# Optimization experiments

Hardware: AMD Instinct MI355X
Metric: run time of the kernel (lower is better)

Reference implementation:

```python
import jax, jax.numpy as jnp
import numpy as np
from jax import lax

V, D, L, H = 8000, 512, 8, 8
B, PROMPT, NEW = 16, 64, 16
T = PROMPT + NEW
PAD, EOS = 0, 3
HD = D // H


def setup_inputs() -> dict:
    key = jax.random.key(0)
    ks = jax.random.split(key, 10)
    s = 0.02
    p = {}
    p['wte'] = jax.random.normal(ks[0], (V, D), jnp.float32) * s
    p['wpe'] = jax.random.normal(ks[1], (T, D), jnp.float32) * s
    p['ln1_w'] = jnp.ones((L, D), jnp.float32)
    p['ln1_b'] = jnp.zeros((L, D), jnp.float32)
    p['qkv_w'] = jax.random.normal(ks[2], (L, D, 3 * D), jnp.float32) * s
    p['qkv_b'] = jnp.zeros((L, 3 * D), jnp.float32)
    p['ao_w'] = jax.random.normal(ks[3], (L, D, D), jnp.float32) * s
    p['ao_b'] = jnp.zeros((L, D), jnp.float32)
    p['ln2_w'] = jnp.ones((L, D), jnp.float32)
    p['ln2_b'] = jnp.zeros((L, D), jnp.float32)
    p['fc_w'] = jax.random.normal(ks[4], (L, D, 4 * D), jnp.float32) * s
    p['fc_b'] = jnp.zeros((L, 4 * D), jnp.float32)
    p['pr_w'] = jax.random.normal(ks[5], (L, 4 * D, D), jnp.float32) * s
    p['pr_b'] = jnp.zeros((L, D), jnp.float32)
    p['lnf_w'] = jnp.ones((D,), jnp.float32)
    p['lnf_b'] = jnp.zeros((D,), jnp.float32)
    p['lm_w'] = jax.random.normal(ks[6], (D, V), jnp.float32) * s
    prompt = jax.random.randint(ks[7], (B, PROMPT), 4, V).astype(jnp.int32)
    p['input_ids'] = jnp.concatenate([prompt, jnp.full((B, NEW), PAD, jnp.int32)], axis=1)
    p['attention_mask'] = jnp.broadcast_to((jnp.arange(T) < PROMPT).astype(jnp.int32), (B, T))
    p['max_new_tokens'] = NEW
    return p


def _ln(x, w, b):
    m = x.mean(-1, keepdims=True)
    v = ((x - m) ** 2).mean(-1, keepdims=True)
    return (x - m) / jnp.sqrt(v + 1e-5) * w + b


def reference(wte, wpe, ln1_w, ln1_b, qkv_w, qkv_b, ao_w, ao_b, ln2_w, ln2_b,
              fc_w, fc_b, pr_w, pr_b, lnf_w, lnf_b, lm_w,
              input_ids, attention_mask, max_new_tokens):
    Bsz, Tlen = input_ids.shape
    causal = jnp.tril(jnp.ones((Tlen, Tlen), bool))
    bidx = jnp.arange(Bsz)
    layer_params = (ln1_w, ln1_b, qkv_w, qkv_b, ao_w, ao_b, ln2_w, ln2_b, fc_w, fc_b, pr_w, pr_b)
    scale = 1.0 / np.sqrt(HD).astype(np.float32)

    def fwd(ids, msk):
        # Full dense forward over the whole (padded) prefix, as the teacher does each step.
        x = wte[ids] + wpe[None, :Tlen]
        bias = jnp.where(causal[None, None] & (msk[:, None, None, :] > 0), 0.0, -1e9)
        def block(x, p):
            l1w, l1b, qw, qb, aw, ab, l2w, l2b, fw, fb, pw, pb = p
            h = _ln(x, l1w, l1b)
            qkv = h @ qw + qb                                  # [B,T,3D]
            q, k, v = jnp.split(qkv, 3, axis=-1)
            def heads(t):
                return t.reshape(Bsz, Tlen, H, HD).transpose(0, 2, 1, 3)
            q, k, v = heads(q), heads(k), heads(v)
            s = jnp.einsum('bhqd,bhkd->bhqk', q, k) * scale + bias
            o = jnp.einsum('bhqk,bhkd->bhqd', jax.nn.softmax(s, axis=-1), v)
            o = o.transpose(0, 2, 1, 3).reshape(Bsz, Tlen, D)
            x = x + o @ aw + ab
            h2 = _ln(x, l2w, l2b)
            x = x + jax.nn.gelu(h2 @ fw + fb) @ pw + pb
            return x, None
        x, _ = lax.scan(block, x, layer_params)
        x = _ln(x, lnf_w, lnf_b)
        return x @ lm_w                                        # [B,T,V]

    lengths = attention_mask.sum(-1).astype(jnp.int32)
    carry0 = (input_ids, attention_mask, lengths,
              jnp.zeros(Bsz, bool), jnp.zeros(Bsz, jnp.float32), jnp.zeros(Bsz, jnp.float32))

    def step(carry, _):
        ids, msk, lens, fin, csum, ccnt = carry
        logits = fwd(ids, msk)
        last = jnp.clip(lens - 1, 0, Tlen - 1)
        sl = logits[bidx, last].astype(jnp.float32)            # [B,V]
        probs = jax.nn.softmax(sl, axis=-1)
        top_id = jnp.argmax(sl, axis=-1).astype(jnp.int32)
        top_p = jnp.max(probs, axis=-1)
        active = (~fin) & (lens < Tlen)
        csum = csum + jnp.where(active, top_p, 0.0)
        ccnt = ccnt + active.astype(jnp.float32)
        is_end = (top_id == EOS) | (top_id == PAD)
        write = active & (~is_end)
        pos = jnp.clip(lens, 0, Tlen - 1)
        ids = ids.at[bidx, pos].set(jnp.where(write, top_id, ids[bidx, pos]))
        msk = msk.at[bidx, pos].set(jnp.where(write, 1, msk[bidx, pos]))
        lens = lens + write.astype(jnp.int32)
        fin = fin | (active & is_end)
        tok = jnp.where(write, top_id, PAD)                    # generated token this step (PAD if none)
        return (ids, msk, lens, fin, csum, ccnt), tok

    carry, toks = lax.scan(step, carry0, None, length=max_new_tokens)
    _, _, _, _, csum, ccnt = carry
    generated = toks.T                                         # [B, max_new_tokens]
    confidences = csum / jnp.maximum(ccnt, 1.0)
    return generated, confidences
```

## Files before the change

### kernel.cpp

```cpp
#include <hip/hip_runtime.h>
#include <math.h>

#define VOCAB 8000
#define DIM 512
#define NLAYER 8
#define NHEAD 8
#define BATCH 16
#define TMAX 80
#define PROMPT_LEN 64
#define NNEW 16
#define HEADD 64
#define ATT_SCALE 0.125f

#define SRC_PLAIN 0
#define SRC_LN 1
#define SRC_GELU 2

__device__ __forceinline__ float gelu_f(float x) {
  return 0.5f * x * (1.0f + tanhf(0.7978845608028654f * (x + 0.044715f * x * x * x)));
}

__global__ void k_init(const int* __restrict__ ids_in, const int* __restrict__ mask_in,
                       int* __restrict__ ids, int* __restrict__ lens, int* __restrict__ fin,
                       float* __restrict__ csum, float* __restrict__ ccnt) {
  int tid = threadIdx.x;
  for (int i = tid; i < BATCH * TMAX; i += blockDim.x) ids[i] = ids_in[i];
  if (tid < BATCH) {
    int s = 0;
    for (int t = 0; t < TMAX; ++t) s += mask_in[tid * TMAX + t];
    lens[tid] = s;
    fin[tid] = 0;
    csum[tid] = 0.f;
    ccnt[tid] = 0.f;
  }
}

__global__ void k_embed_prefill(const int* __restrict__ ids, const float* __restrict__ wte,
                                const float* __restrict__ wpe, float* __restrict__ x) {
  int bt = blockIdx.x;
  int b = bt / PROMPT_LEN, t = bt % PROMPT_LEN;
  int tok = ids[b * TMAX + t];
  for (int d = threadIdx.x; d < DIM; d += blockDim.x)
    x[(size_t)bt * DIM + d] = wte[(size_t)tok * DIM + d] + wpe[(size_t)t * DIM + d];
}

__global__ void k_layernorm(const float* __restrict__ x, const float* __restrict__ w,
                            const float* __restrict__ b, float* __restrict__ out) {
  int row = blockIdx.x;
  int tid = threadIdx.x;
  const float* xr = x + (size_t)row * DIM;
  __shared__ float red[256];
  float v0 = xr[tid], v1 = xr[tid + 256];
  red[tid] = v0 + v1;
  __syncthreads();
  for (int s = 128; s > 0; s >>= 1) {
    if (tid < s) red[tid] += red[tid + s];
    __syncthreads();
  }
  float mean = red[0] * (1.0f / DIM);
  __syncthreads();
  float d0 = v0 - mean, d1 = v1 - mean;
  red[tid] = d0 * d0 + d1 * d1;
  __syncthreads();
  for (int s = 128; s > 0; s >>= 1) {
    if (tid < s) red[tid] += red[tid + s];
    __syncthreads();
  }
  float rstd = 1.0f / sqrtf(red[0] * (1.0f / DIM) + 1e-5f);
  out[(size_t)row * DIM + tid] = d0 * rstd * w[tid] + b[tid];
  out[(size_t)row * DIM + tid + 256] = d1 * rstd * w[tid + 256] + b[tid + 256];
}

template <int MODE>
__global__ __launch_bounds__(256) void gemm_kernel(const float* __restrict__ A,
                                                   const float* __restrict__ W,
                                                   const float* __restrict__ bias,
                                                   const float* __restrict__ res,
                                                   float* __restrict__ C, int M, int N, int K,
                                                   float* __restrict__ kcT,
                                                   float* __restrict__ vc) {
  const int BM = 64, BN = 64, BK = 16;
  __shared__ float As[BK][BM + 4];
  __shared__ float Ws[BK][BN];
  int tid = threadIdx.x;
  int bm = blockIdx.y * BM, bn = blockIdx.x * BN;
  int tr = tid / 16, tc = tid % 16;
  float acc[4][4];
#pragma unroll
  for (int i = 0; i < 4; i++)
#pragma unroll
    for (int j = 0; j < 4; j++) acc[i][j] = 0.f;

  for (int k0 = 0; k0 < K; k0 += BK) {
    for (int i = tid; i < BM * BK; i += 256) {
      int m = i / BK, kk = i % BK;
      As[kk][m] = A[(size_t)(bm + m) * K + k0 + kk];
    }
    for (int i = tid; i < BK * BN; i += 256) {
      int kk = i / BN, n = i % BN;
      Ws[kk][n] = W[(size_t)(k0 + kk) * N + bn + n];
    }
    __syncthreads();
#pragma unroll
    for (int kk = 0; kk < BK; ++kk) {
      float a[4], w[4];
#pragma unroll
      for (int i = 0; i < 4; i++) a[i] = As[kk][tr * 4 + i];
#pragma unroll
      for (int j = 0; j < 4; j++) w[j] = Ws[kk][tc * 4 + j];
#pragma unroll
      for (int i = 0; i < 4; i++)
#pragma unroll
        for (int j = 0; j < 4; j++) acc[i][j] += a[i] * w[j];
    }
    __syncthreads();
  }
#pragma unroll
  for (int i = 0; i < 4; i++) {
    int m = bm + tr * 4 + i;
#pragma unroll
    for (int j = 0; j < 4; j++) {
      int n = bn + tc * 4 + j;
      float v = acc[i][j] + (bias ? bias[n] : 0.f);
      if (MODE == 1) v = gelu_f(v);
      if (MODE == 2) v += res[(size_t)m * N + n];
      if (MODE == 3) {
        int b = m >> 6, t = m & 63;
        if (n < DIM) {
          C[(size_t)m * N + n] = v;
        } else if (n < 2 * DIM) {
          int dd = n - DIM;
          kcT[((size_t)(b * NHEAD + (dd >> 6)) * HEADD + (dd & 63)) * TMAX + t] = v;
        } else {
          int dd = n - 2 * DIM;
          vc[((size_t)(b * NHEAD + (dd >> 6)) * TMAX + t) * HEADD + (dd & 63)] = v;
        }
      } else {
        C[(size_t)m * N + n] = v;
      }
    }
  }
}

__global__ void k_attn_prefill(const float* __restrict__ qkv, const float* __restrict__ kcT,
                               const float* __restrict__ vc, float* __restrict__ o) {
  int blk = blockIdx.x;
  int q = blk % PROMPT_LEN;
  int bh = blk / PROMPT_LEN;
  int h = bh % NHEAD, b = bh / NHEAD;
  int tid = threadIdx.x;
  __shared__ float qs[HEADD];
  __shared__ float ps[PROMPT_LEN];
  qs[tid] = qkv[(size_t)(b * PROMPT_LEN + q) * 3 * DIM + h * HEADD + tid];
  __syncthreads();
  const float* kbT = kcT + (size_t)(b * NHEAD + h) * HEADD * TMAX;
  const float* vb = vc + (size_t)(b * NHEAD + h) * TMAX * HEADD;
  float s = -1e30f;
  if (tid <= q) {
    float a = 0.f;
    for (int d = 0; d < HEADD; ++d) a += qs[d] * kbT[d * TMAX + tid];
    s = a * ATT_SCALE;
  }
  float mx = s;
  for (int off = 32; off > 0; off >>= 1) mx = fmaxf(mx, __shfl_xor(mx, off));
  float e = (tid <= q) ? expf(s - mx) : 0.f;
  float sum = e;
  for (int off = 32; off > 0; off >>= 1) sum += __shfl_xor(sum, off);
  ps[tid] = e / sum;
  __syncthreads();
  float acc = 0.f;
  for (int t = 0; t <= q; ++t) acc += ps[t] * vb[t * HEADD + tid];
  o[(size_t)(b * PROMPT_LEN + q) * DIM + h * HEADD + tid] = acc;
}

__global__ void k_embed0(const int* __restrict__ ids, const int* __restrict__ lens,
                         const float* __restrict__ wte, const float* __restrict__ wpe,
                         float* __restrict__ xdT) {
  int b = blockIdx.x;
  int p = lens[b] - 1;
  if (p < 0) p = 0;
  if (p > TMAX - 1) p = TMAX - 1;
  int tok = ids[b * TMAX + p];
  for (int d = threadIdx.x; d < DIM; d += blockDim.x)
    xdT[(size_t)d * BATCH + b] = wte[(size_t)tok * DIM + d] + wpe[(size_t)p * DIM + d];
}

template <int KB, int SRC, int P, int LAYOUT, bool BIAS, bool XDW, int N, int K>
__global__ __launch_bounds__(512) void k_skinny(const float* __restrict__ src,
                                                const float* __restrict__ parts,
                                                const float* __restrict__ lnw,
                                                const float* __restrict__ lnb,
                                                const float* __restrict__ bias,
                                                const float* __restrict__ W,
                                                float* __restrict__ out,
                                                float* __restrict__ xdout) {
  constexpr int KRANGE = K / KB;
  constexpr int SROWS = (SRC == SRC_LN) ? K : KRANGE;
  __shared__ float sm[SROWS * BATCH];
  __shared__ float wsum[8][BATCH];
  __shared__ float wss[8][BATCH];
  __shared__ float smean[BATCH], srstd[BATCH];
  const int tid = threadIdx.x;
  const int base_row = (SRC == SRC_LN) ? 0 : blockIdx.y * KRANGE;

  {
    const float4* s4 = (const float4*)src;
    float4* d4 = (float4*)sm;
    constexpr int NF4 = SROWS * BATCH / 4;
    for (int i = tid; i < NF4; i += 512) {
      int gi = base_row * (BATCH / 4) + i;
      float4 v;
      if (SRC == SRC_GELU) {
        v = make_float4(0.f, 0.f, 0.f, 0.f);
      } else {
        v = s4[gi];
      }
#pragma unroll
      for (int p = 0; p < P; ++p) {
        const float4* p4 = (const float4*)(parts + (size_t)p * K * BATCH);
        float4 t = p4[gi];
        v.x += t.x;
        v.y += t.y;
        v.z += t.z;
        v.w += t.w;
      }
      if (SRC == SRC_GELU) {
        v.x = gelu_f(v.x);
        v.y = gelu_f(v.y);
        v.z = gelu_f(v.z);
        v.w = gelu_f(v.w);
      }
      if (XDW) {
        if (blockIdx.x == 0 && blockIdx.y == 0) ((float4*)xdout)[gi] = v;
      }
      d4[i] = v;
    }
  }
  if (SRC == SRC_LN) {
    __syncthreads();
    float s = 0.f, ss = 0.f;
#pragma unroll
    for (int j = 0; j < 16; ++j) {
      float v = sm[tid + 512 * j];
      s += v;
      ss += v * v;
    }
    s += __shfl_xor(s, 16);
    ss += __shfl_xor(ss, 16);
    s += __shfl_xor(s, 32);
    ss += __shfl_xor(ss, 32);
    int lane0 = tid & 63, w0 = tid >> 6;
    if (lane0 < BATCH) {
      wsum[w0][lane0] = s;
      wss[w0][lane0] = ss;
    }
    __syncthreads();
    if (tid < BATCH) {
      float ts = 0.f, tss = 0.f;
#pragma unroll
      for (int ww = 0; ww < 8; ++ww) {
        ts += wsum[ww][tid];
        tss += wss[ww][tid];
      }
      float m = ts * (1.0f / K);
      float var = tss * (1.0f / K) - m * m;
      smean[tid] = m;
      srstd[tid] = 1.0f / sqrtf(var + 1e-5f);
    }
    __syncthreads();
    float mb = smean[tid & 15];
    float rb = srstd[tid & 15];
#pragma unroll
    for (int j = 0; j < 16; ++j) {
      int idx = tid + 512 * j;
      int k = idx >> 4;
      sm[idx] = (sm[idx] - mb) * rb * lnw[k] + lnb[k];
    }
  }
  __syncthreads();

  const int lane = tid & 63;
  const int w = tid >> 6;
  const int bw = w & 1;
  const int kw = w >> 1;
  constexpr int KCH = KRANGE / 4;
  const int col = blockIdx.x * 64 + lane;
  const float* Wp = W + (size_t)(blockIdx.y * KRANGE + kw * KCH) * N + col;
  const int fbase = ((SRC == SRC_LN) ? blockIdx.y * KRANGE : 0) + kw * KCH;
  float acc[8];
#pragma unroll
  for (int i = 0; i < 8; ++i) acc[i] = 0.f;
  for (int k = 0; k < KCH; k += 8) {
    float wv[8];
#pragma unroll
    for (int u = 0; u < 8; ++u) wv[u] = Wp[(size_t)(k + u) * N];
#pragma unroll
    for (int u = 0; u < 8; ++u) {
      const float4* a4 = (const float4*)&sm[(fbase + k + u) * BATCH + bw * 8];
      float4 A0 = a4[0], A1 = a4[1];
      acc[0] = fmaf(A0.x, wv[u], acc[0]);
      acc[1] = fmaf(A0.y, wv[u], acc[1]);
      acc[2] = fmaf(A0.z, wv[u], acc[2]);
      acc[3] = fmaf(A0.w, wv[u], acc[3]);
      acc[4] = fmaf(A1.x, wv[u], acc[4]);
      acc[5] = fmaf(A1.y, wv[u], acc[5]);
      acc[6] = fmaf(A1.z, wv[u], acc[6]);
      acc[7] = fmaf(A1.w, wv[u], acc[7]);
    }
  }
  __syncthreads();
#pragma unroll
  for (int i = 0; i < 8; ++i) sm[(w * 8 + i) * 64 + lane] = acc[i];
  __syncthreads();
  for (int o = tid; o < BATCH * 64; o += 512) {
    int b, gn_l;
    if (LAYOUT == 1) {
      b = o & 15;
      gn_l = o >> 4;
    } else {
      b = o >> 6;
      gn_l = o & 63;
    }
    int bw2 = b >> 3, bi = b & 7;
    float v = 0.f;
#pragma unroll
    for (int k2 = 0; k2 < 4; ++k2) v += sm[(((k2 * 2 + bw2) * 8) + bi) * 64 + gn_l];
    int gn = blockIdx.x * 64 + gn_l;
    if (BIAS && blockIdx.y == 0) v += bias[gn];
    if (KB == 1 && LAYOUT == 0)
      out[(size_t)b * N + gn] = v;
    else if (LAYOUT == 0)
      out[((size_t)blockIdx.y * BATCH + b) * N + gn] = v;
    else
      out[(size_t)blockIdx.y * N * BATCH + (size_t)gn * BATCH + b] = v;
  }
}

__global__ void k_attn_decode(const float* __restrict__ qp, const int* __restrict__ lens,
                              float* __restrict__ kcT, float* __restrict__ vc,
                              float* __restrict__ ot) {
  int h = blockIdx.x % NHEAD, b = blockIdx.x / NHEAD;
  int d = threadIdx.x;
  int p = lens[b] - 1;
  if (p < 0) p = 0;
  if (p > TMAX - 1) p = TMAX - 1;
  const float* q0 = qp + (size_t)b * 3 * DIM + h * HEADD;
  const float* q1 = qp + (size_t)BATCH * 3 * DIM + (size_t)b * 3 * DIM + h * HEADD;
  float qv = q0[d] + q1[d];
  float kself = q0[DIM + d] + q1[DIM + d];
  float vself = q0[2 * DIM + d] + q1[2 * DIM + d];
  float* kT = kcT + (size_t)(b * NHEAD + h) * HEADD * TMAX;
  float* vb = vc + (size_t)(b * NHEAD + h) * TMAX * HEADD;
  kT[d * TMAX + p] = kself;
  vb[p * HEADD + d] = vself;
  __shared__ float qs[HEADD];
  __shared__ float ps[TMAX];
  qs[d] = qv;
  __syncthreads();
  float pd = qv * kself;
  for (int off = 32; off > 0; off >>= 1) pd += __shfl_xor(pd, off);
  float selfdot = pd * ATT_SCALE;
  float s0 = -1e30f, s1 = -1e30f;
  int t1 = d + 64;
  if (d < p) {
    float a = 0.f;
    for (int dd = 0; dd < HEADD; ++dd) a += qs[dd] * kT[dd * TMAX + d];
    s0 = a * ATT_SCALE;
  } else if (d == p) {
    s0 = selfdot;
  }
  if (t1 < p) {
    float a = 0.f;
    for (int dd = 0; dd < HEADD; ++dd) a += qs[dd] * kT[dd * TMAX + t1];
    s1 = a * ATT_SCALE;
  } else if (t1 == p) {
    s1 = selfdot;
  }
  float mx = fmaxf(s0, s1);
  for (int off = 32; off > 0; off >>= 1) mx = fmaxf(mx, __shfl_xor(mx, off));
  float e0 = (d <= p) ? expf(s0 - mx) : 0.f;
  float e1 = (t1 <= p) ? expf(s1 - mx) : 0.f;
  float sum = e0 + e1;
  for (int off = 32; off > 0; off >>= 1) sum += __shfl_xor(sum, off);
  float inv = 1.f / sum;
  ps[d] = e0 * inv;
  if (d < TMAX - 64) ps[t1] = e1 * inv;
  __syncthreads();
  float acc = 0.f;
  for (int t = 0; t < p; ++t) acc += ps[t] * vb[t * HEADD + d];
  acc += ps[p] * vself;
  ot[(size_t)(h * HEADD + d) * BATCH + b] = acc;
}

__global__ __launch_bounds__(512) void k_lnf(const float* __restrict__ xd,
                                             const float* __restrict__ parts,
                                             const float* __restrict__ lnw,
                                             const float* __restrict__ lnb,
                                             float* __restrict__ At) {
  __shared__ float sm[DIM * BATCH];
  __shared__ float wsum[8][BATCH];
  __shared__ float wss[8][BATCH];
  __shared__ float smean[BATCH], srstd[BATCH];
  const int tid = threadIdx.x;
  {
    const float4* s4 = (const float4*)xd;
    float4* d4 = (float4*)sm;
    for (int i = tid; i < DIM * BATCH / 4; i += 512) {
      float4 v = s4[i];
#pragma unroll
      for (int p = 0; p < 4; ++p) {
        const float4* p4 = (const float4*)(parts + (size_t)p * DIM * BATCH);
        float4 t = p4[i];
        v.x += t.x;
        v.y += t.y;
        v.z += t.z;
        v.w += t.w;
      }
      d4[i] = v;
    }
  }
  __syncthreads();
  float s = 0.f, ss = 0.f;
#pragma unroll
  for (int j = 0; j < 16; ++j) {
    float v = sm[tid + 512 * j];
    s += v;
    ss += v * v;
  }
  s += __shfl_xor(s, 16);
  ss += __shfl_xor(ss, 16);
  s += __shfl_xor(s, 32);
  ss += __shfl_xor(ss, 32);
  int lane0 = tid & 63, w0 = tid >> 6;
  if (lane0 < BATCH) {
    wsum[w0][lane0] = s;
    wss[w0][lane0] = ss;
  }
  __syncthreads();
  if (tid < BATCH) {
    float ts = 0.f, tss = 0.f;
#pragma unroll
    for (int ww = 0; ww < 8; ++ww) {
      ts += wsum[ww][tid];
      tss += wss[ww][tid];
    }
    float m = ts * (1.0f / DIM);
    float var = tss * (1.0f / DIM) - m * m;
    smean[tid] = m;
    srstd[tid] = 1.0f / sqrtf(var + 1e-5f);
  }
  __syncthreads();
  float mb = smean[tid & 15];
  float rb = srstd[tid & 15];
#pragma unroll
  for (int j = 0; j < 16; ++j) {
    int idx = tid + 512 * j;
    int k = idx >> 4;
    At[idx] = (sm[idx] - mb) * rb * lnw[k] + lnb[k];
  }
}

__global__ void k_update(const float* __restrict__ logits, int* __restrict__ ids,
                         int* __restrict__ lens, int* __restrict__ fin, float* __restrict__ csum,
                         float* __restrict__ ccnt, float* __restrict__ out_gen, int step,
                         const float* __restrict__ wte, const float* __restrict__ wpe,
                         float* __restrict__ xdT) {
  int b = blockIdx.x, tid = threadIdx.x;
  const float* lr = logits + (size_t)b * VOCAB;
  __shared__ float vred[256];
  __shared__ int ired[256];
  __shared__ int sh_tok, sh_pos;
  float best = -1e30f;
  int besti = 0;
  for (int i = tid; i < VOCAB; i += 256) {
    float v = lr[i];
    if (v > best) {
      best = v;
      besti = i;
    }
  }
  vred[tid] = best;
  ired[tid] = besti;
  __syncthreads();
  for (int s = 128; s > 0; s >>= 1) {
    if (tid < s) {
      if (vred[tid + s] > vred[tid] ||
          (vred[tid + s] == vred[tid] && ired[tid + s] < ired[tid])) {
        vred[tid] = vred[tid + s];
        ired[tid] = ired[tid + s];
      }
    }
    __syncthreads();
  }
  float mx = vred[0];
  int top = ired[0];
  __syncthreads();
  float se = 0.f;
  for (int i = tid; i < VOCAB; i += 256) se += expf(lr[i] - mx);
  vred[tid] = se;
  __syncthreads();
  for (int s = 128; s > 0; s >>= 1) {
    if (tid < s) vred[tid] += vred[tid + s];
    __syncthreads();
  }
  if (tid == 0) {
    float top_p = 1.f / vred[0];
    int l = lens[b];
    bool active = (!fin[b]) && (l < TMAX);
    if (active) {
      csum[b] += top_p;
      ccnt[b] += 1.f;
    }
    bool is_end = (top == 3) || (top == 0);
    bool wr = active && !is_end;
    if (wr) {
      ids[b * TMAX + l] = top;
      lens[b] = l + 1;
    }
    if (active && is_end) fin[b] = 1;
    out_gen[b * NNEW + step] = wr ? (float)top : 0.f;
    int l2 = lens[b];
    int pn = l2 - 1;
    if (pn < 0) pn = 0;
    if (pn > TMAX - 1) pn = TMAX - 1;
    sh_pos = pn;
    sh_tok = ids[b * TMAX + pn];
  }
  __syncthreads();
  int tok = sh_tok, pn = sh_pos;
  xdT[(size_t)tid * BATCH + b] = wte[(size_t)tok * DIM + tid] + wpe[(size_t)pn * DIM + tid];
  xdT[(size_t)(tid + 256) * BATCH + b] =
      wte[(size_t)tok * DIM + tid + 256] + wpe[(size_t)pn * DIM + tid + 256];
}

__global__ void k_finalize(const float* __restrict__ csum, const float* __restrict__ ccnt,
                           float* __restrict__ out) {
  int b = threadIdx.x;
  if (b < BATCH) out[BATCH * NNEW + b] = csum[b] / fmaxf(ccnt[b], 1.f);
}

extern "C" void kernel_launch(void* const* d_in, const int* in_sizes, int n_in, void* d_out,
                              int out_size, void* d_ws, size_t ws_size, hipStream_t stream) {
  const float* wte = (const float*)d_in[0];
  const float* wpe = (const float*)d_in[1];
  const float* ln1_w = (const float*)d_in[2];
  const float* ln1_b = (const float*)d_in[3];
  const float* qkv_w = (const float*)d_in[4];
  const float* qkv_b = (const float*)d_in[5];
  const float* ao_w = (const float*)d_in[6];
  const float* ao_b = (const float*)d_in[7];
  const float* ln2_w = (const float*)d_in[8];
  const float* ln2_b = (const float*)d_in[9];
  const float* fc_w = (const float*)d_in[10];
  const float* fc_b = (const float*)d_in[11];
  const float* pr_w = (const float*)d_in[12];
  const float* pr_b = (const float*)d_in[13];
  const float* lnf_w = (const float*)d_in[14];
  const float* lnf_b = (const float*)d_in[15];
  const float* lm_w = (const float*)d_in[16];
  const int* ids_in = (const int*)d_in[17];
  const int* mask_in = (const int*)d_in[18];
  float* out = (float*)d_out;

  char* p = (char*)d_ws;
  auto carve = [&](size_t nbytes) {
    char* r = p;
    p += (nbytes + 255) & ~(size_t)255;
    return (void*)r;
  };
  int* w_ids = (int*)carve(BATCH * TMAX * 4);
  int* w_lens = (int*)carve(BATCH * 4);
  int* w_fin = (int*)carve(BATCH * 4);
  float* w_csum = (float*)carve(BATCH * 4);
  float* w_ccnt = (float*)carve(BATCH * 4);
  float* w_x = (float*)carve((size_t)BATCH * PROMPT_LEN * DIM * 4);
  float* w_h = (float*)carve((size_t)BATCH * PROMPT_LEN * DIM * 4);
  float* w_qkv = (float*)carve((size_t)BATCH * PROMPT_LEN * 3 * DIM * 4);
  float* w_att = (float*)carve((size_t)BATCH * PROMPT_LEN * DIM * 4);
  float* w_mlp = (float*)carve((size_t)BATCH * PROMPT_LEN * 4 * DIM * 4);
  float* w_kc = (float*)carve((size_t)NLAYER * BATCH * NHEAD * TMAX * HEADD * 4);
  float* w_vc = (float*)carve((size_t)NLAYER * BATCH * NHEAD * TMAX * HEADD * 4);
  float* w_xd0 = (float*)carve((size_t)DIM * BATCH * 4);
  float* w_xd1 = (float*)carve((size_t)DIM * BATCH * 4);
  float* w_at = (float*)carve((size_t)DIM * BATCH * 4);
  float* w_ot = (float*)carve((size_t)DIM * BATCH * 4);
  float* w_qkp = (float*)carve((size_t)2 * BATCH * 3 * DIM * 4);
  float* w_aop = (float*)carve((size_t)2 * DIM * BATCH * 4);
  float* w_fcp = (float*)carve((size_t)2 * 4 * DIM * BATCH * 4);
  float* w_prp = (float*)carve((size_t)4 * DIM * BATCH * 4);
  float* w_logits = (float*)carve((size_t)BATCH * VOCAB * 4);

  const int M = BATCH * PROMPT_LEN;
  const size_t kvstride = (size_t)BATCH * NHEAD * TMAX * HEADD;

  k_init<<<1, 256, 0, stream>>>(ids_in, mask_in, w_ids, w_lens, w_fin, w_csum, w_ccnt);
  k_embed_prefill<<<M, 256, 0, stream>>>(w_ids, wte, wpe, w_x);

  for (int l = 0; l < NLAYER; ++l) {
    float* kc = w_kc + (size_t)l * kvstride;
    float* vc = w_vc + (size_t)l * kvstride;
    k_layernorm<<<M, 256, 0, stream>>>(w_x, ln1_w + l * DIM, ln1_b + l * DIM, w_h);
    gemm_kernel<3><<<dim3(3 * DIM / 64, M / 64), 256, 0, stream>>>(
        w_h, qkv_w + (size_t)l * DIM * 3 * DIM, qkv_b + (size_t)l * 3 * DIM, nullptr, w_qkv, M,
        3 * DIM, DIM, kc, vc);
    k_attn_prefill<<<BATCH * NHEAD * PROMPT_LEN, 64, 0, stream>>>(w_qkv, kc, vc, w_att);
    gemm_kernel<2><<<dim3(DIM / 64, M / 64), 256, 0, stream>>>(
        w_att, ao_w + (size_t)l * DIM * DIM, ao_b + (size_t)l * DIM, w_x, w_x, M, DIM, DIM,
        nullptr, nullptr);
    k_layernorm<<<M, 256, 0, stream>>>(w_x, ln2_w + l * DIM, ln2_b + l * DIM, w_h);
    gemm_kernel<1><<<dim3(4 * DIM / 64, M / 64), 256, 0, stream>>>(
        w_h, fc_w + (size_t)l * DIM * 4 * DIM, fc_b + (size_t)l * 4 * DIM, nullptr, w_mlp, M,
        4 * DIM, DIM, nullptr, nullptr);
    gemm_kernel<2><<<dim3(DIM / 64, M / 64), 256, 0, stream>>>(
        w_mlp, pr_w + (size_t)l * 4 * DIM * DIM, pr_b + (size_t)l * DIM, w_x, w_x, M, DIM,
        4 * DIM, nullptr, nullptr);
  }

  k_embed0<<<BATCH, 256, 0, stream>>>(w_ids, w_lens, wte, wpe, w_xd0);

  for (int s = 0; s < NNEW; ++s) {
    for (int l = 0; l < NLAYER; ++l) {
      float* kc = w_kc + (size_t)l * kvstride;
      float* vc = w_vc + (size_t)l * kvstride;
      if (l == 0) {
        k_skinny<2, SRC_LN, 0, 0, true, false, 3 * DIM, DIM>
            <<<dim3(24, 2), 512, 0, stream>>>(w_xd0, nullptr, ln1_w + l * DIM, ln1_b + l * DIM,
                                              qkv_b + (size_t)l * 3 * DIM,
                                              qkv_w + (size_t)l * DIM * 3 * DIM, w_qkp, nullptr);
      } else {
        k_skinny<2, SRC_LN, 4, 0, true, true, 3 * DIM, DIM>
            <<<dim3(24, 2), 512, 0, stream>>>(w_xd1, w_prp, ln1_w + l * DIM, ln1_b + l * DIM,
                                              qkv_b + (size_t)l * 3 * DIM,
                                              qkv_w + (size_t)l * DIM * 3 * DIM, w_qkp, w_xd0);
      }
      k_attn_decode<<<BATCH * NHEAD, 64, 0, stream>>>(w_qkp, w_lens, kc, vc, w_ot);
      k_skinny<2, SRC_PLAIN, 0, 1, true, false, DIM, DIM><<<dim3(8, 2), 512, 0, stream>>>(
          w_ot, nullptr, nullptr, nullptr, ao_b + (size_t)l * DIM, ao_w + (size_t)l * DIM * DIM,
          w_aop, nullptr);
      k_skinny<2, SRC_LN, 2, 1, true, true, 4 * DIM, DIM><<<dim3(32, 2), 512, 0, stream>>>(
          w_xd0, w_aop, ln2_w + l * DIM, ln2_b + l * DIM, fc_b + (size_t)l * 4 * DIM,
          fc_w + (size_t)l * DIM * 4 * DIM, w_fcp, w_xd1);
      k_skinny<4, SRC_GELU, 2, 1, true, false, DIM, 4 * DIM><<<dim3(8, 4), 512, 0, stream>>>(
          nullptr, w_fcp, nullptr, nullptr, pr_b + (size_t)l * DIM,
          pr_w + (size_t)l * 4 * DIM * DIM, w_prp, nullptr);
    }
    k_lnf<<<1, 512, 0, stream>>>(w_xd1, w_prp, lnf_w, lnf_b, w_at);
    k_skinny<1, SRC_PLAIN, 0, 0, false, false, VOCAB, DIM><<<dim3(VOCAB / 64, 1), 512, 0, stream>>>(
        w_at, nullptr, nullptr, nullptr, nullptr, lm_w, w_logits, nullptr);
    k_update<<<BATCH, 256, 0, stream>>>(w_logits, w_ids, w_lens, w_fin, w_csum, w_ccnt, out, s,
                                        wte, wpe, w_xd0);
  }
  k_finalize<<<1, 64, 0, stream>>>(w_csum, w_ccnt, out);
}
```

Baseline: 12.21 ms.

## Fuse decode loop into persistent kernel with atomic grid barriers

Replaces the roughly 100 per-step decode kernel launches with one persistent 128-block kernel. Stages are separated by a software grid barrier built on an atomic counter. Final layernorm is folded into the LM-head GEMM, and attention packs 8 heads per block. This removes launch and inter-kernel gaps, but relies on all 128 blocks being co-resident and adds barrier spin cost.

Result: slower. 21.81 ms (+78.7%).

```diff
diff --git a/kernel.cpp b/kernel.cpp
--- a/kernel.cpp
+++ b/kernel.cpp
@@ -16,15 +16,19 @@
 #define SRC_LN 1
 #define SRC_GELU 2
 
+#define GRIDN 128
+
 __device__ __forceinline__ float gelu_f(float x) {
   return 0.5f * x * (1.0f + tanhf(0.7978845608028654f * (x + 0.044715f * x * x * x)));
 }
 
 __global__ void k_init(const int* __restrict__ ids_in, const int* __restrict__ mask_in,
                        int* __restrict__ ids, int* __restrict__ lens, int* __restrict__ fin,
-                       float* __restrict__ csum, float* __restrict__ ccnt) {
+                       float* __restrict__ csum, float* __restrict__ ccnt,
+                       unsigned long long* __restrict__ bar) {
   int tid = threadIdx.x;
   for (int i = tid; i < BATCH * TMAX; i += blockDim.x) ids[i] = ids_in[i];
+  if (tid == 0) *bar = 0ull;
   if (tid < BATCH) {
     int s = 0;
     for (int t = 0; t < TMAX; ++t) s += mask_in[tid * TMAX + t];
@@ -173,35 +177,55 @@
   o[(size_t)(b * PROMPT_LEN + q) * DIM + h * HEADD + tid] = acc;
 }
 
-__global__ void k_embed0(const int* __restrict__ ids, const int* __restrict__ lens,
-                         const float* __restrict__ wte, const float* __restrict__ wpe,
-                         float* __restrict__ xdT) {
-  int b = blockIdx.x;
-  int p = lens[b] - 1;
-  if (p < 0) p = 0;
-  if (p > TMAX - 1) p = TMAX - 1;
-  int tok = ids[b * TMAX + p];
-  for (int d = threadIdx.x; d < DIM; d += blockDim.x)
-    xdT[(size_t)d * BATCH + b] = wte[(size_t)tok * DIM + d] + wpe[(size_t)p * DIM + d];
+
+struct SmGemm {
+  float sm[DIM * BATCH];
+  float wsum[8][BATCH];
+  float wss[8][BATCH];
+  float smean[BATCH], srstd[BATCH];
+};
+struct SmAttn {
+  float qs[8][HEADD];
+  float ps[8][TMAX];
+};
+struct SmUpd {
+  float vred[512];
+  int ired[512];
+  int sh_tok, sh_pos;
+};
+union SmAll {
+  SmGemm g;
+  SmAttn a;
+  SmUpd u;
+};
+
+__device__ __forceinline__ void gsync(unsigned long long* bar) {
+  __syncthreads();
+  if (threadIdx.x == 0) {
+    unsigned long long arr =
+        __hip_atomic_fetch_add(bar, 1ull, __ATOMIC_RELEASE, __HIP_MEMORY_SCOPE_AGENT);
+    unsigned long long target = (arr / GRIDN + 1ull) * (unsigned long long)GRIDN;
+    while (__hip_atomic_load(bar, __ATOMIC_RELAXED, __HIP_MEMORY_SCOPE_AGENT) < target)
+      __builtin_amdgcn_s_sleep(2);
+    __threadfence();
+  }
+  __syncthreads();
 }
 
 template <int KB, int SRC, int P, int LAYOUT, bool BIAS, bool XDW, int N, int K>
-__global__ __launch_bounds__(512) void k_skinny(const float* __restrict__ src,
-                                                const float* __restrict__ parts,
-                                                const float* __restrict__ lnw,
-                                                const float* __restrict__ lnb,
-                                                const float* __restrict__ bias,
-                                                const float* __restrict__ W,
-                                                float* __restrict__ out,
-                                                float* __restrict__ xdout) {
+__device__ __forceinline__ void skinny_stage(SmGemm& S, int bx, int by,
+                                             const float* __restrict__ src,
+                                             const float* __restrict__ parts,
+                                             const float* __restrict__ lnw,
+                                             const float* __restrict__ lnb,
+                                             const float* __restrict__ bias,
+                                             const float* __restrict__ W, float* __restrict__ out,
+                                             float* __restrict__ xdout) {
   constexpr int KRANGE = K / KB;
   constexpr int SROWS = (SRC == SRC_LN) ? K : KRANGE;
-  __shared__ float sm[SROWS * BATCH];
-  __shared__ float wsum[8][BATCH];
-  __shared__ float wss[8][BATCH];
-  __shared__ float smean[BATCH], srstd[BATCH];
+  float* sm = S.sm;
   const int tid = threadIdx.x;
-  const int base_row = (SRC == SRC_LN) ? 0 : blockIdx.y * KRANGE;
+  const int base_row = (SRC == SRC_LN) ? 0 : by * KRANGE;
 
   {
     const float4* s4 = (const float4*)src;
@@ -231,7 +255,7 @@
         v.w = gelu_f(v.w);
       }
       if (XDW) {
-        if (blockIdx.x == 0 && blockIdx.y == 0) ((float4*)xdout)[gi] = v;
+        if (bx == 0 && by == 0) ((float4*)xdout)[gi] = v;
       }
       d4[i] = v;
     }
@@ -251,25 +275,25 @@
     ss += __shfl_xor(ss, 32);
     int lane0 = tid & 63, w0 = tid >> 6;
     if (lane0 < BATCH) {
-      wsum[w0][lane0] = s;
-      wss[w0][lane0] = ss;
+      S.wsum[w0][lane0] = s;
+      S.wss[w0][lane0] = ss;
     }
     __syncthreads();
     if (tid < BATCH) {
       float ts = 0.f, tss = 0.f;
 #pragma unroll
       for (int ww = 0; ww < 8; ++ww) {
-        ts += wsum[ww][tid];
-        tss += wss[ww][tid];
+        ts += S.wsum[ww][tid];
+        tss += S.wss[ww][tid];
       }
       float m = ts * (1.0f / K);
       float var = tss * (1.0f / K) - m * m;
-      smean[tid] = m;
-      srstd[tid] = 1.0f / sqrtf(var + 1e-5f);
-    }
-    __syncthreads();
-    float mb = smean[tid & 15];
-    float rb = srstd[tid & 15];
+      S.smean[tid] = m;
+      S.srstd[tid] = 1.0f / sqrtf(var + 1e-5f);
+    }
+    __syncthreads();
+    float mb = S.smean[tid & 15];
+    float rb = S.srstd[tid & 15];
 #pragma unroll
     for (int j = 0; j < 16; ++j) {
       int idx = tid + 512 * j;
@@ -284,9 +308,9 @@
   const int bw = w & 1;
   const int kw = w >> 1;
   constexpr int KCH = KRANGE / 4;
-  const int col = blockIdx.x * 64 + lane;
-  const float* Wp = W + (size_t)(blockIdx.y * KRANGE + kw * KCH) * N + col;
-  const int fbase = ((SRC == SRC_LN) ? blockIdx.y * KRANGE : 0) + kw * KCH;
+  const int col = bx * 64 + lane;
+  const float* Wp = W + (size_t)(by * KRANGE + kw * KCH) * N + col;
+  const int fbase = ((SRC == SRC_LN) ? by * KRANGE : 0) + kw * KCH;
   float acc[8];
 #pragma unroll
   for (int i = 0; i < 8; ++i) acc[i] = 0.f;
@@ -325,22 +349,25 @@
     float v = 0.f;
 #pragma unroll
     for (int k2 = 0; k2 < 4; ++k2) v += sm[(((k2 * 2 + bw2) * 8) + bi) * 64 + gn_l];
-    int gn = blockIdx.x * 64 + gn_l;
-    if (BIAS && blockIdx.y == 0) v += bias[gn];
+    int gn = bx * 64 + gn_l;
+    if (BIAS && by == 0) v += bias[gn];
     if (KB == 1 && LAYOUT == 0)
       out[(size_t)b * N + gn] = v;
     else if (LAYOUT == 0)
-      out[((size_t)blockIdx.y * BATCH + b) * N + gn] = v;
+      out[((size_t)by * BATCH + b) * N + gn] = v;
     else
-      out[(size_t)blockIdx.y * N * BATCH + (size_t)gn * BATCH + b] = v;
-  }
-}
-
-__global__ void k_attn_decode(const float* __restrict__ qp, const int* __restrict__ lens,
-                              float* __restrict__ kcT, float* __restrict__ vc,
-                              float* __restrict__ ot) {
-  int h = blockIdx.x % NHEAD, b = blockIdx.x / NHEAD;
-  int d = threadIdx.x;
+      out[(size_t)by * N * BATCH + (size_t)gn * BATCH + b] = v;
+  }
+}
+
+__device__ __forceinline__ void attn_stage(SmAttn& S, int blk, const float* __restrict__ qp,
+                                           const int* __restrict__ lens, float* __restrict__ kcT,
+                                           float* __restrict__ vc, float* __restrict__ ot) {
+  const int tid = threadIdx.x;
+  const int d = tid & 63;
+  const int wv = tid >> 6;
+  const int bh = blk * 8 + wv;
+  const int h = bh % NHEAD, b = bh / NHEAD;
   int p = lens[b] - 1;
   if (p < 0) p = 0;
   if (p > TMAX - 1) p = TMAX - 1;
@@ -349,12 +376,12 @@
   float qv = q0[d] + q1[d];
   float kself = q0[DIM + d] + q1[DIM + d];
   float vself = q0[2 * DIM + d] + q1[2 * DIM + d];
-  float* kT = kcT + (size_t)(b * NHEAD + h) * HEADD * TMAX;
-  float* vb = vc + (size_t)(b * NHEAD + h) * TMAX * HEADD;
+  float* kT = kcT + (size_t)bh * HEADD * TMAX;
+  float* vb = vc + (size_t)bh * TMAX * HEADD;
   kT[d * TMAX + p] = kself;
   vb[p * HEADD + d] = vself;
-  __shared__ float qs[HEADD];
-  __shared__ float ps[TMAX];
+  float* qs = S.qs[wv];
+  float* ps = S.ps[wv];
   qs[d] = qv;
   __syncthreads();
   float pd = qv * kself;
@@ -392,119 +419,48 @@
   ot[(size_t)(h * HEADD + d) * BATCH + b] = acc;
 }
 
-__global__ __launch_bounds__(512) void k_lnf(const float* __restrict__ xd,
-                                             const float* __restrict__ parts,
-                                             const float* __restrict__ lnw,
-                                             const float* __restrict__ lnb,
-                                             float* __restrict__ At) {
-  __shared__ float sm[DIM * BATCH];
-  __shared__ float wsum[8][BATCH];
-  __shared__ float wss[8][BATCH];
-  __shared__ float smean[BATCH], srstd[BATCH];
+__device__ __forceinline__ void update_stage(SmUpd& S, int b, const float* __restrict__ logits,
+                                             int* ids, int* lens, int* fin, float* csum,
+                                             float* ccnt, float* out_gen, int step,
+                                             const float* __restrict__ wte,
+                                             const float* __restrict__ wpe, float* xdT) {
   const int tid = threadIdx.x;
-  {
-    const float4* s4 = (const float4*)xd;
-    float4* d4 = (float4*)sm;
-    for (int i = tid; i < DIM * BATCH / 4; i += 512) {
-      float4 v = s4[i];
-#pragma unroll
-      for (int p = 0; p < 4; ++p) {
-        const float4* p4 = (const float4*)(parts + (size_t)p * DIM * BATCH);
-        float4 t = p4[i];
-        v.x += t.x;
-        v.y += t.y;
-        v.z += t.z;
-        v.w += t.w;
-      }
-      d4[i] = v;
-    }
-  }
-  __syncthreads();
-  float s = 0.f, ss = 0.f;
-#pragma unroll
-  for (int j = 0; j < 16; ++j) {
-    float v = sm[tid + 512 * j];
-    s += v;
-    ss += v * v;
-  }
-  s += __shfl_xor(s, 16);
-  ss += __shfl_xor(ss, 16);
-  s += __shfl_xor(s, 32);
-  ss += __shfl_xor(ss, 32);
-  int lane0 = tid & 63, w0 = tid >> 6;
-  if (lane0 < BATCH) {
-    wsum[w0][lane0] = s;
-    wss[w0][lane0] = ss;
-  }
-  __syncthreads();
-  if (tid < BATCH) {
-    float ts = 0.f, tss = 0.f;
-#pragma unroll
-    for (int ww = 0; ww < 8; ++ww) {
-      ts += wsum[ww][tid];
-      tss += wss[ww][tid];
-    }
-    float m = ts * (1.0f / DIM);
-    float var = tss * (1.0f / DIM) - m * m;
-    smean[tid] = m;
-    srstd[tid] = 1.0f / sqrtf(var + 1e-5f);
-  }
-  __syncthreads();
-  float mb = smean[tid & 15];
-  float rb = srstd[tid & 15];
-#pragma unroll
-  for (int j = 0; j < 16; ++j) {
-    int idx = tid + 512 * j;
-    int k = idx >> 4;
-    At[idx] = (sm[idx] - mb) * rb * lnw[k] + lnb[k];
-  }
-}
-
-__global__ void k_update(const float* __restrict__ logits, int* __restrict__ ids,
-                         int* __restrict__ lens, int* __restrict__ fin, float* __restrict__ csum,
-                         float* __restrict__ ccnt, float* __restrict__ out_gen, int step,
-                         const float* __restrict__ wte, const float* __restrict__ wpe,
-                         float* __restrict__ xdT) {
-  int b = blockIdx.x, tid = threadIdx.x;
   const float* lr = logits + (size_t)b * VOCAB;
-  __shared__ float vred[256];
-  __shared__ int ired[256];
-  __shared__ int sh_tok, sh_pos;
   float best = -1e30f;
   int besti = 0;
-  for (int i = tid; i < VOCAB; i += 256) {
+  for (int i = tid; i < VOCAB; i += 512) {
     float v = lr[i];
     if (v > best) {
       best = v;
       besti = i;
     }
   }
-  vred[tid] = best;
-  ired[tid] = besti;
-  __syncthreads();
-  for (int s = 128; s > 0; s >>= 1) {
+  S.vred[tid] = best;
+  S.ired[tid] = besti;
+  __syncthreads();
+  for (int s = 256; s > 0; s >>= 1) {
     if (tid < s) {
-      if (vred[tid + s] > vred[tid] ||
-          (vred[tid + s] == vred[tid] && ired[tid + s] < ired[tid])) {
-        vred[tid] = vred[tid + s];
-        ired[tid] = ired[tid + s];
-      }
-    }
-    __syncthreads();
-  }
-  float mx = vred[0];
-  int top = ired[0];
+      if (S.vred[tid + s] > S.vred[tid] ||
+          (S.vred[tid + s] == S.vred[tid] && S.ired[tid + s] < S.ired[tid])) {
+        S.vred[tid] = S.vred[tid + s];
+        S.ired[tid] = S.ired[tid + s];
+      }
+    }
+    __syncthreads();
+  }
+  float mx = S.vred[0];
+  int top = S.ired[0];
   __syncthreads();
   float se = 0.f;
-  for (int i = tid; i < VOCAB; i += 256) se += expf(lr[i] - mx);
-  vred[tid] = se;
-  __syncthreads();
-  for (int s = 128; s > 0; s >>= 1) {
-    if (tid < s) vred[tid] += vred[tid + s];
+  for (int i = tid; i < VOCAB; i += 512) se += expf(lr[i] - mx);
+  S.vred[tid] = se;
+  __syncthreads();
+  for (int s = 256; s > 0; s >>= 1) {
+    if (tid < s) S.vred[tid] += S.vred[tid + s];
     __syncthreads();
   }
   if (tid == 0) {
-    float top_p = 1.f / vred[0];
+    float top_p = 1.f / S.vred[0];
     int l = lens[b];
     bool active = (!fin[b]) && (l < TMAX);
     if (active) {
@@ -523,20 +479,84 @@
     int pn = l2 - 1;
     if (pn < 0) pn = 0;
     if (pn > TMAX - 1) pn = TMAX - 1;
-    sh_pos = pn;
-    sh_tok = ids[b * TMAX + pn];
-  }
-  __syncthreads();
-  int tok = sh_tok, pn = sh_pos;
+    S.sh_pos = pn;
+    S.sh_tok = ids[b * TMAX + pn];
+  }
+  __syncthreads();
+  int tok = S.sh_tok, pn = S.sh_pos;
   xdT[(size_t)tid * BATCH + b] = wte[(size_t)tok * DIM + tid] + wpe[(size_t)pn * DIM + tid];
-  xdT[(size_t)(tid + 256) * BATCH + b] =
-      wte[(size_t)tok * DIM + tid + 256] + wpe[(size_t)pn * DIM + tid + 256];
-}
-
-__global__ void k_finalize(const float* __restrict__ csum, const float* __restrict__ ccnt,
-                           float* __restrict__ out) {
-  int b = threadIdx.x;
-  if (b < BATCH) out[BATCH * NNEW + b] = csum[b] / fmaxf(ccnt[b], 1.f);
+}
+
+struct DecArgs {
+  const float *wte, *wpe, *ln1_w, *ln1_b, *qkv_w, *qkv_b, *ao_w, *ao_b, *ln2_w, *ln2_b;
+  const float *fc_w, *fc_b, *pr_w, *pr_b, *lnf_w, *lnf_b, *lm_w;
+  int *ids, *lens, *fin;
+  float *csum, *ccnt;
+  float *kc, *vc;
+  float *xd0, *xd1, *ot, *qkp, *aop, *fcp, *prp, *logits;
+  float* out;
+  unsigned long long* bar;
+};
+
+__global__ __launch_bounds__(512) void k_decode(DecArgs a) {
+  __shared__ SmAll sm;
+  const int blk = blockIdx.x;
+  const int tid = threadIdx.x;
+  const size_t kvstride = (size_t)BATCH * NHEAD * TMAX * HEADD;
+
+  if (blk < BATCH) {
+    int b = blk;
+    int p = a.lens[b] - 1;
+    if (p < 0) p = 0;
+    if (p > TMAX - 1) p = TMAX - 1;
+    int tok = a.ids[b * TMAX + p];
+    a.xd0[(size_t)tid * BATCH + b] = a.wte[(size_t)tok * DIM + tid] + a.wpe[(size_t)p * DIM + tid];
+  }
+  gsync(a.bar);
+
+  for (int s = 0; s < NNEW; ++s) {
+    for (int l = 0; l < NLAYER; ++l) {
+      float* kc = a.kc + (size_t)l * kvstride;
+      float* vc = a.vc + (size_t)l * kvstride;
+      if (blk < 48) {
+        if (l == 0)
+          skinny_stage<2, SRC_LN, 0, 0, true, false, 3 * DIM, DIM>(
+              sm.g, blk % 24, blk / 24, a.xd0, nullptr, a.ln1_w + l * DIM, a.ln1_b + l * DIM,
+              a.qkv_b + (size_t)l * 3 * DIM, a.qkv_w + (size_t)l * DIM * 3 * DIM, a.qkp, nullptr);
+        else
+          skinny_stage<2, SRC_LN, 4, 0, true, true, 3 * DIM, DIM>(
+              sm.g, blk % 24, blk / 24, a.xd1, a.prp, a.ln1_w + l * DIM, a.ln1_b + l * DIM,
+              a.qkv_b + (size_t)l * 3 * DIM, a.qkv_w + (size_t)l * DIM * 3 * DIM, a.qkp, a.xd0);
+      }
+      gsync(a.bar);
+      if (blk < 16) attn_stage(sm.a, blk, a.qkp, a.lens, kc, vc, a.ot);
+      gsync(a.bar);
+      if (blk < 16)
+        skinny_stage<2, SRC_PLAIN, 0, 1, true, false, DIM, DIM>(
+            sm.g, blk % 8, blk / 8, a.ot, nullptr, nullptr, nullptr, a.ao_b + (size_t)l * DIM,
+            a.ao_w + (size_t)l * DIM * DIM, a.aop, nullptr);
+      gsync(a.bar);
+      if (blk < 64)
+        skinny_stage<2, SRC_LN, 2, 1, true, true, 4 * DIM, DIM>(
+            sm.g, blk % 32, blk / 32, a.xd0, a.aop, a.ln2_w + l * DIM, a.ln2_b + l * DIM,
+            a.fc_b + (size_t)l * 4 * DIM, a.fc_w + (size_t)l * DIM * 4 * DIM, a.fcp, a.xd1);
+      gsync(a.bar);
+      if (blk < 32)
+        skinny_stage<4, SRC_GELU, 2, 1, true, false, DIM, 4 * DIM>(
+            sm.g, blk % 8, blk / 8, nullptr, a.fcp, nullptr, nullptr, a.pr_b + (size_t)l * DIM,
+            a.pr_w + (size_t)l * 4 * DIM * DIM, a.prp, nullptr);
+      gsync(a.bar);
+    }
+    if (blk < VOCAB / 64)
+      skinny_stage<1, SRC_LN, 4, 0, false, false, VOCAB, DIM>(
+          sm.g, blk, 0, a.xd1, a.prp, a.lnf_w, a.lnf_b, nullptr, a.lm_w, a.logits, nullptr);
+    gsync(a.bar);
+    if (blk < BATCH)
+      update_stage(sm.u, blk, a.logits, a.ids, a.lens, a.fin, a.csum, a.ccnt, a.out, s, a.wte,
+                   a.wpe, a.xd0);
+    gsync(a.bar);
+  }
+  if (blk == 0 && tid < BATCH) a.out[BATCH * NNEW + tid] = a.csum[tid] / fmaxf(a.ccnt[tid], 1.f);
 }
 
 extern "C" void kernel_launch(void* const* d_in, const int* in_sizes, int n_in, void* d_out,
@@ -582,18 +602,18 @@
   float* w_vc = (float*)carve((size_t)NLAYER * BATCH * NHEAD * TMAX * HEADD * 4);
   float* w_xd0 = (float*)carve((size_t)DIM * BATCH * 4);
   float* w_xd1 = (float*)carve((size_t)DIM * BATCH * 4);
-  float* w_at = (float*)carve((size_t)DIM * BATCH * 4);
   float* w_ot = (float*)carve((size_t)DIM * BATCH * 4);
   float* w_qkp = (float*)carve((size_t)2 * BATCH * 3 * DIM * 4);
   float* w_aop = (float*)carve((size_t)2 * DIM * BATCH * 4);
   float* w_fcp = (float*)carve((size_t)2 * 4 * DIM * BATCH * 4);
   float* w_prp = (float*)carve((size_t)4 * DIM * BATCH * 4);
   float* w_logits = (float*)carve((size_t)BATCH * VOCAB * 4);
+  unsigned long long* w_bar = (unsigned long long*)carve(256);
 
   const int M = BATCH * PROMPT_LEN;
   const size_t kvstride = (size_t)BATCH * NHEAD * TMAX * HEADD;
 
-  k_init<<<1, 256, 0, stream>>>(ids_in, mask_in, w_ids, w_lens, w_fin, w_csum, w_ccnt);
+  k_init<<<1, 256, 0, stream>>>(ids_in, mask_in, w_ids, w_lens, w_fin, w_csum, w_ccnt, w_bar);
   k_embed_prefill<<<M, 256, 0, stream>>>(w_ids, wte, wpe, w_x);
 
   for (int l = 0; l < NLAYER; ++l) {
@@ -616,39 +636,40 @@
         4 * DIM, nullptr, nullptr);
   }
 
-  k_embed0<<<BATCH, 256, 0, stream>>>(w_ids, w_lens, wte, wpe, w_xd0);
-
-  for (int s = 0; s < NNEW; ++s) {
-    for (int l = 0; l < NLAYER; ++l) {
-      float* kc = w_kc + (size_t)l * kvstride;
-      float* vc = w_vc + (size_t)l * kvstride;
-      if (l == 0) {
-        k_skinny<2, SRC_LN, 0, 0, true, false, 3 * DIM, DIM>
-            <<<dim3(24, 2), 512, 0, stream>>>(w_xd0, nullptr, ln1_w + l * DIM, ln1_b + l * DIM,
-                                              qkv_b + (size_t)l * 3 * DIM,
-                                              qkv_w + (size_t)l * DIM * 3 * DIM, w_qkp, nullptr);
-      } else {
-        k_skinny<2, SRC_LN, 4, 0, true, true, 3 * DIM, DIM>
-            <<<dim3(24, 2), 512, 0, stream>>>(w_xd1, w_prp, ln1_w + l * DIM, ln1_b + l * DIM,
-                                              qkv_b + (size_t)l * 3 * DIM,
-                                              qkv_w + (size_t)l * DIM * 3 * DIM, w_qkp, w_xd0);
-      }
-      k_attn_decode<<<BATCH * NHEAD, 64, 0, stream>>>(w_qkp, w_lens, kc, vc, w_ot);
-      k_skinny<2, SRC_PLAIN, 0, 1, true, false, DIM, DIM><<<dim3(8, 2), 512, 0, stream>>>(
-          w_ot, nullptr, nullptr, nullptr, ao_b + (size_t)l * DIM, ao_w + (size_t)l * DIM * DIM,
-          w_aop, nullptr);
-      k_skinny<2, SRC_LN, 2, 1, true, true, 4 * DIM, DIM><<<dim3(32, 2), 512, 0, stream>>>(
-          w_xd0, w_aop, ln2_w + l * DIM, ln2_b + l * DIM, fc_b + (size_t)l * 4 * DIM,
-          fc_w + (size_t)l * DIM * 4 * DIM, w_fcp, w_xd1);
-      k_skinny<4, SRC_GELU, 2, 1, true, false, DIM, 4 * DIM><<<dim3(8, 4), 512, 0, stream>>>(
-          nullptr, w_fcp, nullptr, nullptr, pr_b + (size_t)l * DIM,
-          pr_w + (size_t)l * 4 * DIM * DIM, w_prp, nullptr);
-    }
-    k_lnf<<<1, 512, 0, stream>>>(w_xd1, w_prp, lnf_w, lnf_b, w_at);
-    k_skinny<1, SRC_PLAIN, 0, 0, false, false, VOCAB, DIM><<<dim3(VOCAB / 64, 1), 512, 0, stream>>>(
-        w_at, nullptr, nullptr, nullptr, nullptr, lm_w, w_logits, nullptr);
-    k_update<<<BATCH, 256, 0, stream>>>(w_logits, w_ids, w_lens, w_fin, w_csum, w_ccnt, out, s,
-                                        wte, wpe, w_xd0);
-  }
-  k_finalize<<<1, 64, 0, stream>>>(w_csum, w_ccnt, out);
-}
+  DecArgs da;
+  da.wte = wte;
+  da.wpe = wpe;
+  da.ln1_w = ln1_w;
+  da.ln1_b = ln1_b;
+  da.qkv_w = qkv_w;
+  da.qkv_b = qkv_b;
+  da.ao_w = ao_w;
+  da.ao_b = ao_b;
+  da.ln2_w = ln2_w;
+  da.ln2_b = ln2_b;
+  da.fc_w = fc_w;
+  da.fc_b = fc_b;
+  da.pr_w = pr_w;
+  da.pr_b = pr_b;
+  da.lnf_w = lnf_w;
+  da.lnf_b = lnf_b;
+  da.lm_w = lm_w;
+  da.ids = w_ids;
+  da.lens = w_lens;
+  da.fin = w_fin;
+  da.csum = w_csum;
+  da.ccnt = w_ccnt;
+  da.kc = w_kc;
+  da.vc = w_vc;
+  da.xd0 = w_xd0;
+  da.xd1 = w_xd1;
+  da.ot = w_ot;
+  da.qkp = w_qkp;
+  da.aop = w_aop;
+  da.fcp = w_fcp;
+  da.prp = w_prp;
+  da.logits = w_logits;
+  da.out = out;
+  da.bar = w_bar;
+  k_decode<<<GRIDN, 512, 0, stream>>>(da);
+}
```
